# Optimization experiments

Measured on AMD Instinct MI355X. Metric: run time of the kernel, lower is better.

Reference implementation:

```python
import jax, jax.numpy as jnp
import numpy as np

EPS = 1e-8
B, ST, SL, V, D, H, L, NC = 64, 512, 64, 32000, 256, 256, 1, 20


def lstm_scan(x, Wih, Whh, bih, bhh):
    # x: (B, T, Din) -> (hs (B,T,H), h_last (B,H)); PyTorch gate order [i,f,g,o]
    nb = x.shape[0]
    nh = Whh.shape[1]
    bias = bih + bhh
    def step(carry, xt):
        h, c = carry
        g = xt @ Wih.T + h @ Whh.T + bias
        i, f, gg, o = jnp.split(g, 4, axis=-1)
        c = jax.nn.sigmoid(f) * c + jax.nn.sigmoid(i) * jnp.tanh(gg)
        h = jax.nn.sigmoid(o) * jnp.tanh(c)
        return (h, c), h
    h0 = jnp.zeros((nb, nh), x.dtype)
    (hT, _), hs = jax.lax.scan(step, (h0, h0), jnp.swapaxes(x, 0, 1))
    return jnp.swapaxes(hs, 0, 1), hT


def bilstm(x, Wih_f, Whh_f, bih_f, bhh_f, Wih_b, Whh_b, bih_b, bhh_b):
    hs_f, hT_f = lstm_scan(x, Wih_f, Whh_f, bih_f, bhh_f)
    hs_br, hT_b = lstm_scan(x[:, ::-1], Wih_b, Whh_b, bih_b, bhh_b)
    return hs_f, hs_br[:, ::-1], hT_f, hT_b


def mp_match(v1, v2, w):
    # v1: (B,S,H); v2: (B,H) (broadcast over seq, as in torch.stack([v2]*seq));
    # w: (l,H). Returns (B,S,l): cosine over hidden dim of (w*v1, w*v2).
    a = v1[:, :, None, :] * w[None, None]          # (B,S,l,H)
    bmat = v2[:, None, None, :] * w[None, None]    # (B,1,l,H)
    num = jnp.sum(a * bmat, -1)
    den = jnp.linalg.norm(a, axis=-1) * jnp.linalg.norm(bmat, axis=-1)
    return num / jnp.maximum(den, EPS)


def setup_inputs() -> dict:
    key = jax.random.key(0)
    ks = jax.random.split(key, 16)
    def rn(k, shp, scale=0.05):
        return (jax.random.normal(k, shp) * scale).astype(jnp.float32)
    inp = {
        "text": jax.random.randint(ks[0], (B, ST), 0, V),
        "label_meaning": jax.random.randint(ks[1], (B, SL), 0, V),
        "emb": rn(ks[2], (V, D), 1.0),
        "ctx_Wih_f": rn(ks[3], (4 * H, D)),
        "ctx_Whh_f": rn(ks[4], (4 * H, H)),
        "ctx_bih_f": jnp.zeros((4 * H,), jnp.float32),
        "ctx_bhh_f": jnp.zeros((4 * H,), jnp.float32),
        "ctx_Wih_b": rn(ks[5], (4 * H, D)),
        "ctx_Whh_b": rn(ks[6], (4 * H, H)),
        "ctx_bih_b": jnp.zeros((4 * H,), jnp.float32),
        "ctx_bhh_b": jnp.zeros((4 * H,), jnp.float32),
        "mp_w1": rn(ks[7], (L, H), 1.0),
        "mp_w2": rn(ks[8], (L, H), 1.0),
        "agg_Wih_f": rn(ks[9], (4 * H, 2 * L)),
        "agg_Whh_f": rn(ks[10], (4 * H, H)),
        "agg_bih_f": jnp.zeros((4 * H,), jnp.float32),
        "agg_bhh_f": jnp.zeros((4 * H,), jnp.float32),
        "agg_Wih_b": rn(ks[11], (4 * H, 2 * L)),
        "agg_Whh_b": rn(ks[12], (4 * H, H)),
        "agg_bih_b": jnp.zeros((4 * H,), jnp.float32),
        "agg_bhh_b": jnp.zeros((4 * H,), jnp.float32),
        "fc1_W": (jax.random.uniform(ks[13], (2 * H, 4 * H), minval=-0.005, maxval=0.005)).astype(jnp.float32),
        "fc1_b": jnp.zeros((2 * H,), jnp.float32),
        "fc2_W": (jax.random.uniform(ks[14], (NC, 2 * H), minval=-0.005, maxval=0.005)).astype(jnp.float32),
        "fc2_b": jnp.zeros((NC,), jnp.float32),
    }
    return inp


def reference(text, label_meaning, emb, ctx_Wih_f, ctx_Whh_f, ctx_bih_f, ctx_bhh_f,
              ctx_Wih_b, ctx_Whh_b, ctx_bih_b, ctx_bhh_b, mp_w1, mp_w2,
              agg_Wih_f, agg_Whh_f, agg_bih_f, agg_bhh_f,
              agg_Wih_b, agg_Whh_b, agg_bih_b, agg_bhh_b,
              fc1_W, fc1_b, fc2_W, fc2_b):
    p = emb[text]           # (B,ST,D)
    h = emb[label_meaning]  # (B,SL,D)
    cp_f, cp_b, _, _ = bilstm(p, ctx_Wih_f, ctx_Whh_f, ctx_bih_f, ctx_bhh_f,
                              ctx_Wih_b, ctx_Whh_b, ctx_bih_b, ctx_bhh_b)
    ch_f, ch_b, _, _ = bilstm(h, ctx_Wih_f, ctx_Whh_f, ctx_bih_f, ctx_bhh_f,
                              ctx_Wih_b, ctx_Whh_b, ctx_bih_b, ctx_bhh_b)
    # full-matching: premise vs last fw / first bw hidden of hypothesis (and vice versa)
    mv_p = jnp.concatenate([mp_match(cp_f, ch_f[:, -1], mp_w1),
                            mp_match(cp_b, ch_b[:, 0], mp_w2)], axis=2)  # (B,ST,2l)
    mv_h = jnp.concatenate([mp_match(ch_f, cp_f[:, -1], mp_w1),
                            mp_match(ch_b, cp_b[:, 0], mp_w2)], axis=2)  # (B,SL,2l)
    _, _, pT_f, pT_b = bilstm(mv_p, agg_Wih_f, agg_Whh_f, agg_bih_f, agg_bhh_f,
                              agg_Wih_b, agg_Whh_b, agg_bih_b, agg_bhh_b)
    _, _, hT_f, hT_b = bilstm(mv_h, agg_Wih_f, agg_Whh_f, agg_bih_f, agg_bhh_f,
                              agg_Wih_b, agg_Whh_b, agg_bih_b, agg_bhh_b)
    x = jnp.concatenate([pT_f, pT_b, hT_f, hT_b], axis=1)  # (B, 4H)
    x = jnp.tanh(x @ fc1_W.T + fc1_b)
    return x @ fc2_W.T + fc2_b  # (B, n_class)
```

## Files before the change

### kernel.cpp

```cpp
#include <hip/hip_runtime.h>
#include <math.h>

#define BB 64
#define STT 512
#define SLL 64
#define DD 256
#define HH 256
#define HB 16384

typedef __bf16 v8bf __attribute__((ext_vector_type(8)));
typedef float f32x16 __attribute__((ext_vector_type(16)));

#define MFMA(a, b, c) __builtin_amdgcn_mfma_f32_32x32x16_bf16(a, b, c, 0, 0, 0)

__device__ __forceinline__ float sigm(float x) { return 1.0f / (1.0f + __expf(-x)); }
__device__ __forceinline__ v8bf ldv(const __bf16* p) { return *(const v8bf*)p; }

struct PArgs {
  const __bf16* xhi[4];
  const __bf16* xlo[4];
  const float* mv[4];
  const float* whh[4];
  const float* wih[4];
  const float* bih[4];
  const float* bhh[4];
  float* hs[4];
  __bf16* hxhi[4];
  __bf16* hxlo[4];
  unsigned int* sync;
  int T[4];
  int dir[4];
};

template <int XMODE>
__global__ __launch_bounds__(256, 1) void lstm_persist(PArgs A) {
  const int s = blockIdx.x & 7;
  if (s >= 4) return;
  const int jb = blockIdx.x >> 3;
  const int T = A.T[s];
  const int dir = A.dir[s];
  const int tid = threadIdx.x;
  const int lane = tid & 63;
  const int g = tid >> 6;
  const int l31 = lane & 31;
  const int khalf = (lane >> 5) << 3;
  const int u_base = jb * 32;

  __shared__ float lds_g[4][64][32];
  __shared__ float bias_s[4][32];
  __shared__ float w0_s[4][32];
  __shared__ float w1_s[4][32];

  if (tid < 128) {
    int gg = tid >> 5, uu = tid & 31;
    int row = gg * 256 + u_base + uu;
    bias_s[gg][uu] = A.bih[s][row] + A.bhh[s][row];
    if (XMODE == 1) {
      w0_s[gg][uu] = A.wih[s][row * 2 + 0];
      w1_s[gg][uu] = A.wih[s][row * 2 + 1];
    }
  }

  v8bf whhhi[16], whhlo[16], wihhi[16], wihlo[16];
  {
    const int row = g * 256 + u_base + l31;
    const float* rp = A.whh[s] + (size_t)row * 256 + khalf;
#pragma unroll
    for (int kt = 0; kt < 16; ++kt) {
      float4 q0 = *(const float4*)(rp + kt * 16);
      float4 q1 = *(const float4*)(rp + kt * 16 + 4);
      float vv[8] = {q0.x, q0.y, q0.z, q0.w, q1.x, q1.y, q1.z, q1.w};
#pragma unroll
      for (int e = 0; e < 8; ++e) {
        __bf16 hh = (__bf16)vv[e];
        whhhi[kt][e] = hh;
        whhlo[kt][e] = (__bf16)(vv[e] - (float)hh);
      }
    }
    if (XMODE == 0) {
      const float* rq = A.wih[s] + (size_t)row * 256 + khalf;
#pragma unroll
      for (int kt = 0; kt < 16; ++kt) {
        float4 q0 = *(const float4*)(rq + kt * 16);
        float4 q1 = *(const float4*)(rq + kt * 16 + 4);
        float vv[8] = {q0.x, q0.y, q0.z, q0.w, q1.x, q1.y, q1.z, q1.w};
#pragma unroll
        for (int e = 0; e < 8; ++e) {
          __bf16 hh = (__bf16)vv[e];
          wihhi[kt][e] = hh;
          wihlo[kt][e] = (__bf16)(vv[e] - (float)hh);
        }
      }
    }
  }

  float c[8];
#pragma unroll
  for (int p = 0; p < 8; ++p) c[p] = 0.f;

  const int u = tid & 31, bb0 = tid >> 5;
  unsigned int* ctr = A.sync + s * 64;
  unsigned int* flag = ctr + 32;

  __syncthreads();

  for (int t = 0; t < T; ++t) {
    const __bf16* hp_hi = A.hxhi[s] + ((t + 1) & 1) * HB;
    const __bf16* hp_lo = A.hxlo[s] + ((t + 1) & 1) * HB;
    const __bf16* xr_hi = nullptr;
    const __bf16* xr_lo = nullptr;
    if (XMODE == 0) {
      int m0 = (dir ? (T - 1 - t) : t) * 64;
      xr_hi = A.xhi[s] + (size_t)m0 * 256;
      xr_lo = A.xlo[s] + (size_t)m0 * 256;
    }
    f32x16 acc0 = (f32x16)(0.0f);
    f32x16 acc1 = (f32x16)(0.0f);
#pragma unroll
    for (int kt = 0; kt < 16; ++kt) {
      const int ko = kt * 16 + khalf;
      v8bf ah0 = ldv(hp_hi + (size_t)l31 * 256 + ko);
      v8bf al0 = ldv(hp_lo + (size_t)l31 * 256 + ko);
      v8bf ah1 = ldv(hp_hi + (size_t)(l31 + 32) * 256 + ko);
      v8bf al1 = ldv(hp_lo + (size_t)(l31 + 32) * 256 + ko);
      acc0 = MFMA(ah0, whhhi[kt], acc0);
      acc0 = MFMA(al0, whhhi[kt], acc0);
      acc0 = MFMA(ah0, whhlo[kt], acc0);
      acc1 = MFMA(ah1, whhhi[kt], acc1);
      acc1 = MFMA(al1, whhhi[kt], acc1);
      acc1 = MFMA(ah1, whhlo[kt], acc1);
      if (XMODE == 0) {
        v8bf xh0 = ldv(xr_hi + (size_t)l31 * 256 + ko);
        v8bf xl0 = ldv(xr_lo + (size_t)l31 * 256 + ko);
        v8bf xh1 = ldv(xr_hi + (size_t)(l31 + 32) * 256 + ko);
        v8bf xl1 = ldv(xr_lo + (size_t)(l31 + 32) * 256 + ko);
        acc0 = MFMA(xh0, wihhi[kt], acc0);
        acc0 = MFMA(xl0, wihhi[kt], acc0);
        acc0 = MFMA(xh0, wihlo[kt], acc0);
        acc1 = MFMA(xh1, wihhi[kt], acc1);
        acc1 = MFMA(xl1, wihhi[kt], acc1);
        acc1 = MFMA(xh1, wihlo[kt], acc1);
      }
    }
#pragma unroll
    for (int r = 0; r < 16; ++r) {
      int m = (r & 3) + 8 * (r >> 2) + 4 * (lane >> 5);
      lds_g[g][m][l31] = acc0[r];
      lds_g[g][m + 32][l31] = acc1[r];
    }
    __syncthreads();

    __bf16* ho_hi = A.hxhi[s] + (t & 1) * HB;
    __bf16* ho_lo = A.hxlo[s] + (t & 1) * HB;
    float* hsout = A.hs[s] + (size_t)t * HB;
    const int t_eff = dir ? (T - 1 - t) : t;
#pragma unroll
    for (int p = 0; p < 8; ++p) {
      int b = p * 8 + bb0;
      float g0 = lds_g[0][b][u] + bias_s[0][u];
      float g1 = lds_g[1][b][u] + bias_s[1][u];
      float g2 = lds_g[2][b][u] + bias_s[2][u];
      float g3 = lds_g[3][b][u] + bias_s[3][u];
      if (XMODE == 1) {
        float m0 = A.mv[s][t_eff * 128 + b];
        float m1 = A.mv[s][t_eff * 128 + 64 + b];
        g0 += w0_s[0][u] * m0 + w1_s[0][u] * m1;
        g1 += w0_s[1][u] * m0 + w1_s[1][u] * m1;
        g2 += w0_s[2][u] * m0 + w1_s[2][u] * m1;
        g3 += w0_s[3][u] * m0 + w1_s[3][u] * m1;
      }
      float iv = sigm(g0), fv = sigm(g1), zv = tanhf(g2), ov = sigm(g3);
      float cn = fv * c[p] + iv * zv;
      c[p] = cn;
      float hv = ov * tanhf(cn);
      int ug = u_base + u;
      __bf16 hh = (__bf16)hv;
      ho_hi[b * 256 + ug] = hh;
      ho_lo[b * 256 + ug] = (__bf16)(hv - (float)hh);
      hsout[ug * 64 + b] = hv;
    }
    __syncthreads();

    if (tid == 0) {
      __threadfence();
      unsigned int arrive = atomicAdd(ctr, 1u) + 1u;
      unsigned int want = (unsigned int)(t + 1);
      if (arrive == 8u * want) {
        __hip_atomic_store(flag, want, __ATOMIC_RELEASE, __HIP_MEMORY_SCOPE_AGENT);
      }
      unsigned int v;
      do {
        v = __hip_atomic_load(flag, __ATOMIC_ACQUIRE, __HIP_MEMORY_SCOPE_AGENT);
      } while (v < want);
    }
    __syncthreads();
  }
}

__global__ __launch_bounds__(256) void gather_split(const int* __restrict__ tok,
                                                    const float* __restrict__ emb,
                                                    __bf16* __restrict__ xhi,
                                                    __bf16* __restrict__ xlo, int T) {
  size_t idx = (size_t)blockIdx.x * 256 + threadIdx.x;
  int k = idx & 255;
  size_t m = idx >> 8;
  int b = (int)(m & 63);
  int t = (int)(m >> 6);
  int token = tok[b * T + t];
  float v = emb[(size_t)token * 256 + k];
  __bf16 h = (__bf16)v;
  xhi[idx] = h;
  xlo[idx] = (__bf16)(v - (float)h);
}

__global__ __launch_bounds__(256) void mv_match(const float* __restrict__ hsf,
                                                const float* __restrict__ hsb,
                                                const float* __restrict__ vf,
                                                const float* __restrict__ vb,
                                                const float* __restrict__ w1,
                                                const float* __restrict__ w2,
                                                float* __restrict__ mv, int T) {
  int b = threadIdx.x & 63;
  int t = blockIdx.x * 4 + (threadIdx.x >> 6);
  if (t >= T) return;
  {
    const float* v1 = hsf + (size_t)t * HH * BB;
    float num = 0.f, na = 0.f, nb = 0.f;
    for (int k = 0; k < HH; ++k) {
      float w = w1[k];
      float av = w * v1[k * BB + b];
      float bv = w * vf[k * BB + b];
      num = fmaf(av, bv, num);
      na = fmaf(av, av, na);
      nb = fmaf(bv, bv, nb);
    }
    mv[((size_t)t * 2 + 0) * BB + b] = num / fmaxf(sqrtf(na) * sqrtf(nb), 1e-8f);
  }
  {
    const float* v1 = hsb + (size_t)(T - 1 - t) * HH * BB;
    float num = 0.f, na = 0.f, nb = 0.f;
    for (int k = 0; k < HH; ++k) {
      float w = w2[k];
      float av = w * v1[k * BB + b];
      float bv = w * vb[k * BB + b];
      num = fmaf(av, bv, num);
      na = fmaf(av, av, na);
      nb = fmaf(bv, bv, nb);
    }
    mv[((size_t)t * 2 + 1) * BB + b] = num / fmaxf(sqrtf(na) * sqrtf(nb), 1e-8f);
  }
}

__global__ __launch_bounds__(256) void final_fc(const float* __restrict__ pf,
                                                const float* __restrict__ pb,
                                                const float* __restrict__ hf,
                                                const float* __restrict__ hb,
                                                const float* __restrict__ fc1W,
                                                const float* __restrict__ fc1b,
                                                const float* __restrict__ fc2W,
                                                const float* __restrict__ fc2b,
                                                float* __restrict__ out) {
  __shared__ float xs[1024];
  __shared__ float ys[512];
  int b = blockIdx.x;
  for (int i = threadIdx.x; i < 1024; i += 256) {
    const float* src = (i < 256) ? pf : (i < 512) ? pb : (i < 768) ? hf : hb;
    xs[i] = src[(size_t)(i & 255) * BB + b];
  }
  __syncthreads();
  for (int o = threadIdx.x; o < 512; o += 256) {
    float acc = fc1b[o];
    const float* w = fc1W + (size_t)o * 1024;
#pragma unroll 4
    for (int k = 0; k < 1024; ++k) acc = fmaf(w[k], xs[k], acc);
    ys[o] = tanhf(acc);
  }
  __syncthreads();
  if (threadIdx.x < 20) {
    int o = threadIdx.x;
    float acc = fc2b[o];
    const float* w = fc2W + (size_t)o * 512;
#pragma unroll 4
    for (int k = 0; k < 512; ++k) acc = fmaf(w[k], ys[k], acc);
    out[b * 20 + o] = acc;
  }
}

__global__ void guard_fill(float* out, int n, float v) {
  int i = blockIdx.x * 256 + threadIdx.x;
  if (i < n) out[i] = v;
}

extern "C" void kernel_launch(void* const* d_in, const int* in_sizes, int n_in,
                              void* d_out, int out_size, void* d_ws, size_t ws_size,
                              hipStream_t stream) {
  const int* text = (const int*)d_in[0];
  const int* label = (const int*)d_in[1];
  const float* emb = (const float*)d_in[2];
  const float* cWih_f = (const float*)d_in[3];
  const float* cWhh_f = (const float*)d_in[4];
  const float* cbih_f = (const float*)d_in[5];
  const float* cbhh_f = (const float*)d_in[6];
  const float* cWih_b = (const float*)d_in[7];
  const float* cWhh_b = (const float*)d_in[8];
  const float* cbih_b = (const float*)d_in[9];
  const float* cbhh_b = (const float*)d_in[10];
  const float* w1 = (const float*)d_in[11];
  const float* w2 = (const float*)d_in[12];
  const float* aWih_f = (const float*)d_in[13];
  const float* aWhh_f = (const float*)d_in[14];
  const float* abih_f = (const float*)d_in[15];
  const float* abhh_f = (const float*)d_in[16];
  const float* aWih_b = (const float*)d_in[17];
  const float* aWhh_b = (const float*)d_in[18];
  const float* abih_b = (const float*)d_in[19];
  const float* abhh_b = (const float*)d_in[20];
  const float* fc1W = (const float*)d_in[21];
  const float* fc1b = (const float*)d_in[22];
  const float* fc2W = (const float*)d_in[23];
  const float* fc2b = (const float*)d_in[24];
  float* out = (float*)d_out;

  char* base = (char*)d_ws;
  size_t off = 0;
  auto alloc = [&](size_t bytes) {
    void* p = base + off;
    off = (off + bytes + 255) & ~(size_t)255;
    return p;
  };

  __bf16* xp_hi = (__bf16*)alloc((size_t)STT * 64 * 256 * 2);
  __bf16* xp_lo = (__bf16*)alloc((size_t)STT * 64 * 256 * 2);
  __bf16* xh_hi = (__bf16*)alloc((size_t)SLL * 64 * 256 * 2);
  __bf16* xh_lo = (__bf16*)alloc((size_t)SLL * 64 * 256 * 2);
  float* hs_pf = (float*)alloc((size_t)STT * HB * 4);
  float* hs_pb = (float*)alloc((size_t)STT * HB * 4);
  float* hs_hf = (float*)alloc((size_t)SLL * HB * 4);
  float* hs_hb = (float*)alloc((size_t)SLL * HB * 4);
  float* mv_p = (float*)alloc((size_t)STT * 2 * 64 * 4);
  float* mv_h = (float*)alloc((size_t)SLL * 2 * 64 * 4);
  __bf16* hxbase = (__bf16*)alloc(8 * 4 * HB * sizeof(__bf16));
  unsigned int* syncb = (unsigned int*)alloc(4096);

  if (ws_size < off) {
    guard_fill<<<(out_size + 255) / 256, 256, 0, stream>>>(out, out_size,
                                                           (float)(ws_size >> 20));
    return;
  }

  hipMemsetAsync(hxbase, 0, 8 * 4 * HB * sizeof(__bf16) + 4096, stream);

  gather_split<<<(STT * 64 * 256) / 256, 256, 0, stream>>>(text, emb, xp_hi, xp_lo, STT);
  gather_split<<<(SLL * 64 * 256) / 256, 256, 0, stream>>>(label, emb, xh_hi, xh_lo, SLL);

  PArgs cx;
  for (int s = 0; s < 4; ++s) {
    cx.xhi[s] = (s < 2) ? xp_hi : xh_hi;
    cx.xlo[s] = (s < 2) ? xp_lo : xh_lo;
    cx.mv[s] = nullptr;
    cx.whh[s] = (s & 1) ? cWhh_b : cWhh_f;
    cx.wih[s] = (s & 1) ? cWih_b : cWih_f;
    cx.bih[s] = (s & 1) ? cbih_b : cbih_f;
    cx.bhh[s] = (s & 1) ? cbhh_b : cbhh_f;
    cx.hxhi[s] = hxbase + (size_t)s * 4 * HB;
    cx.hxlo[s] = hxbase + (size_t)s * 4 * HB + 2 * HB;
    cx.T[s] = (s < 2) ? STT : SLL;
    cx.dir[s] = s & 1;
  }
  cx.hs[0] = hs_pf; cx.hs[1] = hs_pb; cx.hs[2] = hs_hf; cx.hs[3] = hs_hb;
  cx.sync = syncb;
  lstm_persist<0><<<64, 256, 0, stream>>>(cx);

  mv_match<<<STT / 4, 256, 0, stream>>>(hs_pf, hs_pb, hs_hf + (size_t)(SLL - 1) * HB,
                                        hs_hb + (size_t)(SLL - 1) * HB, w1, w2, mv_p, STT);
  mv_match<<<SLL / 4, 256, 0, stream>>>(hs_hf, hs_hb, hs_pf + (size_t)(STT - 1) * HB,
                                        hs_pb + (size_t)(STT - 1) * HB, w1, w2, mv_h, SLL);

  PArgs ag;
  for (int s = 0; s < 4; ++s) {
    ag.xhi[s] = nullptr;
    ag.xlo[s] = nullptr;
    ag.mv[s] = (s < 2) ? mv_p : mv_h;
    ag.whh[s] = (s & 1) ? aWhh_b : aWhh_f;
    ag.wih[s] = (s & 1) ? aWih_b : aWih_f;
    ag.bih[s] = (s & 1) ? abih_b : abih_f;
    ag.bhh[s] = (s & 1) ? abhh_b : abhh_f;
    ag.hxhi[s] = hxbase + (size_t)(4 + s) * 4 * HB;
    ag.hxlo[s] = hxbase + (size_t)(4 + s) * 4 * HB + 2 * HB;
    ag.T[s] = (s < 2) ? STT : SLL;
    ag.dir[s] = s & 1;
  }
  ag.hs[0] = hs_pf; ag.hs[1] = hs_pb; ag.hs[2] = hs_hf; ag.hs[3] = hs_hb;
  ag.sync = syncb + 256;
  lstm_persist<1><<<64, 256, 0, stream>>>(ag);

  final_fc<<<BB, 256, 0, stream>>>(hs_pf + (size_t)(STT - 1) * HB,
                                   hs_pb + (size_t)(STT - 1) * HB,
                                   hs_hf + (size_t)(SLL - 1) * HB,
                                   hs_hb + (size_t)(SLL - 1) * HB,
                                   fc1W, fc1b, fc2W, fc2b, out);
}
```

Measured before the change: 18.10 ms.

## Replace counter barrier with per-block flag slots and pack hi/lo hidden state

Replaces the atomic-counter-plus-flag grid barrier with per-block release slots that 64 lanes poll together using __any and s_sleep. The hi/lo bf16 hidden-state halves are packed into one 32-bit word per element and moved with relaxed agent-scope atomics, so each block does a single store per element and fewer loads. The hs layout changes to batch-major, the aggregation LSTM skips hs writes except on the last step, and mv_match and final_fc are updated for the new layout. The aim is lower per-step synchronisation and memory latency on the serial recurrence, at the cost of relying on relaxed atomics plus slot release/acquire for correctness.

Result: slower. 24.91 ms (+37.6%).

```diff
diff --git a/kernel.cpp b/kernel.cpp
--- a/kernel.cpp
+++ b/kernel.cpp
@@ -10,11 +10,15 @@
 
 typedef __bf16 v8bf __attribute__((ext_vector_type(8)));
 typedef float f32x16 __attribute__((ext_vector_type(16)));
+typedef unsigned long long u64;
 
 #define MFMA(a, b, c) __builtin_amdgcn_mfma_f32_32x32x16_bf16(a, b, c, 0, 0, 0)
 
 __device__ __forceinline__ float sigm(float x) { return 1.0f / (1.0f + __expf(-x)); }
 __device__ __forceinline__ v8bf ldv(const __bf16* p) { return *(const v8bf*)p; }
+__device__ __forceinline__ __bf16 bfbits(unsigned short u) {
+  return __builtin_bit_cast(__bf16, u);
+}
 
 struct PArgs {
   const __bf16* xhi[4];
@@ -25,9 +29,8 @@
   const float* bih[4];
   const float* bhh[4];
   float* hs[4];
-  __bf16* hxhi[4];
-  __bf16* hxlo[4];
-  unsigned int* sync;
+  unsigned* hx[4];
+  unsigned* sync;
   int T[4];
   int dir[4];
 };
@@ -99,14 +102,12 @@
   for (int p = 0; p < 8; ++p) c[p] = 0.f;
 
   const int u = tid & 31, bb0 = tid >> 5;
-  unsigned int* ctr = A.sync + s * 64;
-  unsigned int* flag = ctr + 32;
+  unsigned* slots = A.sync + s * 256;
 
   __syncthreads();
 
   for (int t = 0; t < T; ++t) {
-    const __bf16* hp_hi = A.hxhi[s] + ((t + 1) & 1) * HB;
-    const __bf16* hp_lo = A.hxlo[s] + ((t + 1) & 1) * HB;
+    unsigned* hprev = A.hx[s] + ((t + 1) & 1) * HB;
     const __bf16* xr_hi = nullptr;
     const __bf16* xr_lo = nullptr;
     if (XMODE == 0) {
@@ -116,13 +117,34 @@
     }
     f32x16 acc0 = (f32x16)(0.0f);
     f32x16 acc1 = (f32x16)(0.0f);
+    const u64* hq0 = (const u64*)(hprev + (size_t)l31 * 256);
+    const u64* hq1 = (const u64*)(hprev + (size_t)(l31 + 32) * 256);
 #pragma unroll
     for (int kt = 0; kt < 16; ++kt) {
-      const int ko = kt * 16 + khalf;
-      v8bf ah0 = ldv(hp_hi + (size_t)l31 * 256 + ko);
-      v8bf al0 = ldv(hp_lo + (size_t)l31 * 256 + ko);
-      v8bf ah1 = ldv(hp_hi + (size_t)(l31 + 32) * 256 + ko);
-      v8bf al1 = ldv(hp_lo + (size_t)(l31 + 32) * 256 + ko);
+      const int qb = kt * 8 + (khalf >> 1);
+      u64 q0[4], q1[4];
+#pragma unroll
+      for (int e = 0; e < 4; ++e)
+        q0[e] = __hip_atomic_load((const u64*)hq0 + qb + e, __ATOMIC_RELAXED,
+                                  __HIP_MEMORY_SCOPE_AGENT);
+#pragma unroll
+      for (int e = 0; e < 4; ++e)
+        q1[e] = __hip_atomic_load((const u64*)hq1 + qb + e, __ATOMIC_RELAXED,
+                                  __HIP_MEMORY_SCOPE_AGENT);
+      v8bf ah0, al0, ah1, al1;
+#pragma unroll
+      for (int e = 0; e < 4; ++e) {
+        unsigned w0 = (unsigned)q0[e], w1 = (unsigned)(q0[e] >> 32);
+        ah0[2 * e] = bfbits((unsigned short)(w0 & 0xffff));
+        al0[2 * e] = bfbits((unsigned short)(w0 >> 16));
+        ah0[2 * e + 1] = bfbits((unsigned short)(w1 & 0xffff));
+        al0[2 * e + 1] = bfbits((unsigned short)(w1 >> 16));
+        unsigned y0 = (unsigned)q1[e], y1 = (unsigned)(q1[e] >> 32);
+        ah1[2 * e] = bfbits((unsigned short)(y0 & 0xffff));
+        al1[2 * e] = bfbits((unsigned short)(y0 >> 16));
+        ah1[2 * e + 1] = bfbits((unsigned short)(y1 & 0xffff));
+        al1[2 * e + 1] = bfbits((unsigned short)(y1 >> 16));
+      }
       acc0 = MFMA(ah0, whhhi[kt], acc0);
       acc0 = MFMA(al0, whhhi[kt], acc0);
       acc0 = MFMA(ah0, whhlo[kt], acc0);
@@ -130,6 +152,7 @@
       acc1 = MFMA(al1, whhhi[kt], acc1);
       acc1 = MFMA(ah1, whhlo[kt], acc1);
       if (XMODE == 0) {
+        const int ko = kt * 16 + khalf;
         v8bf xh0 = ldv(xr_hi + (size_t)l31 * 256 + ko);
         v8bf xl0 = ldv(xr_lo + (size_t)l31 * 256 + ko);
         v8bf xh1 = ldv(xr_hi + (size_t)(l31 + 32) * 256 + ko);
@@ -150,8 +173,7 @@
     }
     __syncthreads();
 
-    __bf16* ho_hi = A.hxhi[s] + (t & 1) * HB;
-    __bf16* ho_lo = A.hxlo[s] + (t & 1) * HB;
+    unsigned* ho = A.hx[s] + (t & 1) * HB;
     float* hsout = A.hs[s] + (size_t)t * HB;
     const int t_eff = dir ? (T - 1 - t) : t;
 #pragma unroll
@@ -174,24 +196,27 @@
       c[p] = cn;
       float hv = ov * tanhf(cn);
       int ug = u_base + u;
-      __bf16 hh = (__bf16)hv;
-      ho_hi[b * 256 + ug] = hh;
-      ho_lo[b * 256 + ug] = (__bf16)(hv - (float)hh);
-      hsout[ug * 64 + b] = hv;
+      unsigned short hb_ = __builtin_bit_cast(unsigned short, (__bf16)hv);
+      float hif = (float)bfbits(hb_);
+      unsigned short lb_ = __builtin_bit_cast(unsigned short, (__bf16)(hv - hif));
+      unsigned pack = ((unsigned)lb_ << 16) | (unsigned)hb_;
+      __hip_atomic_store(&ho[(size_t)b * 256 + ug], pack, __ATOMIC_RELAXED,
+                         __HIP_MEMORY_SCOPE_AGENT);
+      if (XMODE == 0 || t == T - 1) hsout[(size_t)b * 256 + ug] = hv;
     }
     __syncthreads();
 
-    if (tid == 0) {
-      __threadfence();
-      unsigned int arrive = atomicAdd(ctr, 1u) + 1u;
-      unsigned int want = (unsigned int)(t + 1);
-      if (arrive == 8u * want) {
-        __hip_atomic_store(flag, want, __ATOMIC_RELEASE, __HIP_MEMORY_SCOPE_AGENT);
-      }
-      unsigned int v;
-      do {
-        v = __hip_atomic_load(flag, __ATOMIC_ACQUIRE, __HIP_MEMORY_SCOPE_AGENT);
-      } while (v < want);
+    const unsigned want = (unsigned)(t + 1);
+    if (tid == 0)
+      __hip_atomic_store(&slots[jb * 32], want, __ATOMIC_RELEASE,
+                         __HIP_MEMORY_SCOPE_AGENT);
+    if (tid < 64) {
+      for (;;) {
+        unsigned v = __hip_atomic_load(&slots[(lane & 7) * 32], __ATOMIC_ACQUIRE,
+                                       __HIP_MEMORY_SCOPE_AGENT);
+        if (!__any(v < want)) break;
+        __builtin_amdgcn_s_sleep(2);
+      }
     }
     __syncthreads();
   }
@@ -224,12 +249,14 @@
   int t = blockIdx.x * 4 + (threadIdx.x >> 6);
   if (t >= T) return;
   {
-    const float* v1 = hsf + (size_t)t * HH * BB;
+    const float* v1 = hsf + ((size_t)t * 64 + b) * 256;
+    const float* v2 = vf + (size_t)b * 256;
     float num = 0.f, na = 0.f, nb = 0.f;
+#pragma unroll 4
     for (int k = 0; k < HH; ++k) {
       float w = w1[k];
-      float av = w * v1[k * BB + b];
-      float bv = w * vf[k * BB + b];
+      float av = w * v1[k];
+      float bv = w * v2[k];
       num = fmaf(av, bv, num);
       na = fmaf(av, av, na);
       nb = fmaf(bv, bv, nb);
@@ -237,12 +264,14 @@
     mv[((size_t)t * 2 + 0) * BB + b] = num / fmaxf(sqrtf(na) * sqrtf(nb), 1e-8f);
   }
   {
-    const float* v1 = hsb + (size_t)(T - 1 - t) * HH * BB;
+    const float* v1 = hsb + ((size_t)(T - 1 - t) * 64 + b) * 256;
+    const float* v2 = vb + (size_t)b * 256;
     float num = 0.f, na = 0.f, nb = 0.f;
+#pragma unroll 4
     for (int k = 0; k < HH; ++k) {
       float w = w2[k];
-      float av = w * v1[k * BB + b];
-      float bv = w * vb[k * BB + b];
+      float av = w * v1[k];
+      float bv = w * v2[k];
       num = fmaf(av, bv, num);
       na = fmaf(av, av, na);
       nb = fmaf(bv, bv, nb);
@@ -265,7 +294,7 @@
   int b = blockIdx.x;
   for (int i = threadIdx.x; i < 1024; i += 256) {
     const float* src = (i < 256) ? pf : (i < 512) ? pb : (i < 768) ? hf : hb;
-    xs[i] = src[(size_t)(i & 255) * BB + b];
+    xs[i] = src[(size_t)b * 256 + (i & 255)];
   }
   __syncthreads();
   for (int o = threadIdx.x; o < 512; o += 256) {
@@ -339,8 +368,8 @@
   float* hs_hb = (float*)alloc((size_t)SLL * HB * 4);
   float* mv_p = (float*)alloc((size_t)STT * 2 * 64 * 4);
   float* mv_h = (float*)alloc((size_t)SLL * 2 * 64 * 4);
-  __bf16* hxbase = (__bf16*)alloc(8 * 4 * HB * sizeof(__bf16));
-  unsigned int* syncb = (unsigned int*)alloc(4096);
+  unsigned* hxbase = (unsigned*)alloc((size_t)8 * 2 * HB * 4);
+  unsigned* syncb = (unsigned*)alloc(4096);
 
   if (ws_size < off) {
     guard_fill<<<(out_size + 255) / 256, 256, 0, stream>>>(out, out_size,
@@ -348,7 +377,7 @@
     return;
   }
 
-  hipMemsetAsync(hxbase, 0, 8 * 4 * HB * sizeof(__bf16) + 4096, stream);
+  hipMemsetAsync(hxbase, 0, (size_t)8 * 2 * HB * 4 + 4096, stream);
 
   gather_split<<<(STT * 64 * 256) / 256, 256, 0, stream>>>(text, emb, xp_hi, xp_lo, STT);
   gather_split<<<(SLL * 64 * 256) / 256, 256, 0, stream>>>(label, emb, xh_hi, xh_lo, SLL);
@@ -362,8 +391,7 @@
     cx.wih[s] = (s & 1) ? cWih_b : cWih_f;
     cx.bih[s] = (s & 1) ? cbih_b : cbih_f;
     cx.bhh[s] = (s & 1) ? cbhh_b : cbhh_f;
-    cx.hxhi[s] = hxbase + (size_t)s * 4 * HB;
-    cx.hxlo[s] = hxbase + (size_t)s * 4 * HB + 2 * HB;
+    cx.hx[s] = hxbase + (size_t)s * 2 * HB;
     cx.T[s] = (s < 2) ? STT : SLL;
     cx.dir[s] = s & 1;
   }
@@ -385,13 +413,12 @@
     ag.wih[s] = (s & 1) ? aWih_b : aWih_f;
     ag.bih[s] = (s & 1) ? abih_b : abih_f;
     ag.bhh[s] = (s & 1) ? abhh_b : abhh_f;
-    ag.hxhi[s] = hxbase + (size_t)(4 + s) * 4 * HB;
-    ag.hxlo[s] = hxbase + (size_t)(4 + s) * 4 * HB + 2 * HB;
+    ag.hx[s] = hxbase + (size_t)(4 + s) * 2 * HB;
     ag.T[s] = (s < 2) ? STT : SLL;
     ag.dir[s] = s & 1;
   }
   ag.hs[0] = hs_pf; ag.hs[1] = hs_pb; ag.hs[2] = hs_hf; ag.hs[3] = hs_hb;
-  ag.sync = syncb + 256;
+  ag.sync = syncb + 1024 / sizeof(unsigned) * 1;
   lstm_persist<1><<<64, 256, 0, stream>>>(ag);
 
   final_fc<<<BB, 256, 0, stream>>>(hs_pf + (size_t)(STT - 1) * HB,
```
